# Optimization experiments

Hardware: AMD Instinct MI355X
Metric: run time of the kernel (lower is better)

## Reference

```python
import jax, jax.numpy as jnp
import numpy as np

D = 2048          # n_embd
F = 1408          # moe_inter_dim
E = 8             # n_routed_experts
TOPK = 2          # n_activated_experts
N_SHARED = 2
ROUTE_SCALE = 1.0


def setup_inputs() -> dict:
    key = jax.random.key(0)
    ks = jax.random.split(key, 8)
    s = 0.02
    x = jax.random.normal(ks[0], (2, 1024, D), dtype=jnp.float32)
    gate_w = jax.random.normal(ks[1], (D, E), dtype=jnp.float32) * s
    Fs = F * N_SHARED
    sw1 = jax.random.normal(ks[2], (D, Fs), dtype=jnp.float32) * s
    sw2 = jax.random.normal(ks[3], (Fs, D), dtype=jnp.float32) * s
    sw3 = jax.random.normal(ks[4], (D, Fs), dtype=jnp.float32) * s
    rw1 = jax.random.normal(ks[5], (E, D, F), dtype=jnp.float32) * s
    rw2 = jax.random.normal(ks[6], (E, F, D), dtype=jnp.float32) * s
    rw3 = jax.random.normal(ks[7], (E, D, F), dtype=jnp.float32) * s
    return {"x": x, "gate_w": gate_w, "sw1": sw1, "sw2": sw2, "sw3": sw3,
            "rw1": rw1, "rw2": rw2, "rw3": rw3}


def _swiglu(x, w1, w2, w3):
    return (jax.nn.silu(x @ w1) * (x @ w3)) @ w2


def reference(x, gate_w, sw1, sw2, sw3, rw1, rw2, rw3):
    B, T, _ = x.shape
    xf = x.reshape(-1, D)                       # [N, D]
    N = xf.shape[0]
    # shared experts (always applied)
    y = _swiglu(xf, sw1, sw2, sw3)              # [N, D]
    # gate: softmax scores, top-k (bias is None since n_embd != 7168; n_groups == 1)
    scores = jax.nn.softmax(xf @ gate_w, axis=-1)       # [N, E]
    weights, indices = jax.lax.top_k(scores, TOPK)       # gathered original scores
    weights = weights * ROUTE_SCALE
    # combine weights per (token, expert); zero for unassigned -> same math as
    # the per-expert gather/scatter loop in the original module
    cw = jnp.zeros((N, E), dtype=xf.dtype).at[jnp.arange(N)[:, None], indices].add(weights)
    for e in range(E):  # fixed small structural loop over experts
        h = _swiglu(xf, rw1[e], rw2[e], rw3[e])  # [N, D]
        y = y + cw[:, e:e + 1] * h
    return y.reshape(B, T, D)
```

## Files before the change

### kernel.cpp

```cpp
#include <hip/hip_runtime.h>
#include <hip/hip_bf16.h>
#include <math.h>

#define D_DIM 2048
#define F_DIM 1408
#define FS_DIM 2816
#define E_NUM 8
#define N_TOK 2048

typedef __attribute__((ext_vector_type(8))) short bf16x8;
typedef __attribute__((ext_vector_type(4))) float f32x4;

#define WAITVM(n) asm volatile("s_waitcnt vmcnt(" #n ")" ::: "memory")

__device__ inline short f2bf(float f) {
    __hip_bfloat16 h = __float2bfloat16(f);
    return *reinterpret_cast<short*>(&h);
}
__device__ inline float bf2f(short s) {
    __hip_bfloat16 h; *reinterpret_cast<short*>(&h) = s;
    return __bfloat162float(h);
}
__device__ inline float silu1(float v) { return v / (1.f + expf(-v)); }

__device__ inline void async_copy16(const void* g, void* l) {
    __builtin_amdgcn_global_load_lds(
        (const __attribute__((address_space(1))) void*)g,
        (__attribute__((address_space(3))) void*)l, 16, 0, 0);
}

#define SWZ(r, s) ((((s) ^ (((r) >> 1) & 3)) & 3) << 4)

__device__ inline void t64h(const float* in, short* out, int K, int N,
                            int kt, int nt, float (*tile)[65], int t)
{
    int k0 = kt * 64, n0 = nt * 64;
    int tr = t >> 4, tc4 = (t & 15) * 4;
#pragma unroll
    for (int i = 0; i < 4; ++i) {
        int r = tr + i * 16;
        float4 v = *reinterpret_cast<const float4*>(in + (size_t)(k0 + r) * N + n0 + tc4);
        tile[r][tc4 + 0] = v.x; tile[r][tc4 + 1] = v.y;
        tile[r][tc4 + 2] = v.z; tile[r][tc4 + 3] = v.w;
    }
    __syncthreads();
#pragma unroll
    for (int i = 0; i < 4; ++i) {
        int n = tr + i * 16;
        short4 s4;
        s4.x = f2bf(tile[tc4 + 0][n]);
        s4.y = f2bf(tile[tc4 + 1][n]);
        s4.z = f2bf(tile[tc4 + 2][n]);
        s4.w = f2bf(tile[tc4 + 3][n]);
        *reinterpret_cast<short4*>(out + (size_t)(n0 + n) * K + k0 + tc4) = s4;
    }
}

__global__ __launch_bounds__(256) void prep_kernel(
    const float* __restrict__ x, const float* __restrict__ gw,
    float* __restrict__ assign_w, int* __restrict__ expert_count,
    int* __restrict__ expert_list, short* __restrict__ Xb,
    const float* __restrict__ sw1, short* __restrict__ swt1,
    const float* __restrict__ sw3, short* __restrict__ swt3,
    const float* __restrict__ rw1, short* __restrict__ rwt1,
    const float* __restrict__ rw3, short* __restrict__ rwt3)
{
    __shared__ float tile[64][65];
    int bid = blockIdx.x;
    int tid = threadIdx.x;
    if (bid < 512) {
        int wid = bid * 4 + (tid >> 6);
        int lane = tid & 63;
        const float* xr = x + (size_t)wid * D_DIM;
        float p[E_NUM];
#pragma unroll
        for (int e = 0; e < E_NUM; ++e) p[e] = 0.f;
        for (int d = lane; d < D_DIM; d += 64) {
            float xv = xr[d];
            const float4* g = reinterpret_cast<const float4*>(gw + (size_t)d * E_NUM);
            float4 g0 = g[0], g1 = g[1];
            p[0] = fmaf(xv, g0.x, p[0]); p[1] = fmaf(xv, g0.y, p[1]);
            p[2] = fmaf(xv, g0.z, p[2]); p[3] = fmaf(xv, g0.w, p[3]);
            p[4] = fmaf(xv, g1.x, p[4]); p[5] = fmaf(xv, g1.y, p[5]);
            p[6] = fmaf(xv, g1.z, p[6]); p[7] = fmaf(xv, g1.w, p[7]);
        }
#pragma unroll
        for (int off = 32; off > 0; off >>= 1)
#pragma unroll
            for (int e = 0; e < E_NUM; ++e)
                p[e] += __shfl_xor(p[e], off, 64);
        if (lane == 0) {
            float m = p[0];
#pragma unroll
            for (int e = 1; e < E_NUM; ++e) m = fmaxf(m, p[e]);
            float s = 0.f, pr[E_NUM];
#pragma unroll
            for (int e = 0; e < E_NUM; ++e) { pr[e] = expf(p[e] - m); s += pr[e]; }
            float inv = 1.f / s;
#pragma unroll
            for (int e = 0; e < E_NUM; ++e) pr[e] *= inv;
            int i0 = 0;
#pragma unroll
            for (int e = 1; e < E_NUM; ++e) if (pr[e] > pr[i0]) i0 = e;
            int i1 = (i0 == 0) ? 1 : 0;
#pragma unroll
            for (int e = 0; e < E_NUM; ++e) if (e != i0 && pr[e] > pr[i1]) i1 = e;
            int s0 = wid * 2, s1 = wid * 2 + 1;
            assign_w[s0] = pr[i0];
            assign_w[s1] = pr[i1];
            int p0 = atomicAdd(&expert_count[i0], 1);
            expert_list[i0 * N_TOK + p0] = s0;
            int p1 = atomicAdd(&expert_count[i1], 1);
            expert_list[i1 * N_TOK + p1] = s1;
        }
    } else if (bid < 2560) {
        int i = ((bid - 512) * 256 + tid) * 8;
        float4 v0 = *reinterpret_cast<const float4*>(x + i);
        float4 v1 = *reinterpret_cast<const float4*>(x + i + 4);
        bf16x8 o;
        o[0] = f2bf(v0.x); o[1] = f2bf(v0.y); o[2] = f2bf(v0.z); o[3] = f2bf(v0.w);
        o[4] = f2bf(v1.x); o[5] = f2bf(v1.y); o[6] = f2bf(v1.z); o[7] = f2bf(v1.w);
        *reinterpret_cast<bf16x8*>(Xb + i) = o;
    } else if (bid < 3968) {
        int t = bid - 2560;
        t64h(sw1, swt1, D_DIM, FS_DIM, t % 32, t / 32, tile, tid);
    } else if (bid < 5376) {
        int t = bid - 3968;
        t64h(sw3, swt3, D_DIM, FS_DIM, t % 32, t / 32, tile, tid);
    } else if (bid < 11008) {
        int t = bid - 5376;
        int e = t / 704, r = t % 704;
        t64h(rw1 + (size_t)e * D_DIM * F_DIM, rwt1 + (size_t)e * F_DIM * D_DIM,
             D_DIM, F_DIM, r % 32, r / 32, tile, tid);
    } else {
        int t = bid - 11008;
        int e = t / 704, r = t % 704;
        t64h(rw3 + (size_t)e * D_DIM * F_DIM, rwt3 + (size_t)e * F_DIM * D_DIM,
             D_DIM, F_DIM, r % 32, r / 32, tile, tid);
    }
}

__global__ __launch_bounds__(256) void moe_in_kernel(
    const short* __restrict__ Xb,
    const short* __restrict__ swt1, const short* __restrict__ swt3, short* __restrict__ Hs,
    const short* __restrict__ rwt1, const short* __restrict__ rwt3, short* __restrict__ Hr,
    const int* __restrict__ expert_list, const int* __restrict__ expert_count,
    const float* __restrict__ sw2, short* __restrict__ swt2,
    const float* __restrict__ rw2, short* __restrict__ rwt2)
{
    __shared__ char SMEM[49152];
    int bid = blockIdx.x, tid = threadIdx.x;

    if (bid >= 3584) {
        int t2 = bid - 3584;
        float (*tile)[65] = reinterpret_cast<float (*)[65]>(SMEM);
        if (t2 < 1408) {
            t64h(sw2, swt2, FS_DIM, D_DIM, t2 % 44, t2 / 44, tile, tid);
        } else {
            int r = t2 - 1408;
            int e = r / 704, rr = r % 704;
            t64h(rw2 + (size_t)e * F_DIM * D_DIM, rwt2 + (size_t)e * D_DIM * F_DIM,
                 F_DIM, D_DIM, rr % 22, rr / 22, tile, tid);
        }
        return;
    }

    int xcd = bid & 7, qq = bid >> 3, mtile = qq & 15, gq = qq >> 4;
    int g = gq * 8 + xcd;
    if (g >= 220) return;
    bool gather;
    const short *W1, *W3;
    short* H;
    int ldH, n0, count;
    const int* list = nullptr;
    int m0 = mtile * 128;
    if (g < 44) {
        gather = false; count = N_TOK;
        W1 = swt1; W3 = swt3; H = Hs; ldH = FS_DIM; n0 = g * 64;
    } else {
        int g2 = g - 44, e = g2 / 22;
        n0 = (g2 % 22) * 64;
        gather = true;
        count = expert_count[e];
        if (m0 >= count) return;
        list = expert_list + e * N_TOK;
        W1 = rwt1 + (size_t)e * F_DIM * D_DIM;
        W3 = rwt3 + (size_t)e * F_DIM * D_DIM;
        H = Hr; ldH = F_DIM;
    }

    int l = tid & 63, w = tid >> 6;
    int wm = w >> 1, wn = w & 1, frow = l & 15, fkg = l >> 4;

    const char* aS[2];
#pragma unroll
    for (int j = 0; j < 2; ++j) {
        int u = j * 256 + tid, r = u >> 2, s = u & 3;
        int rr = m0 + r;
        int tok = gather ? ((rr < count) ? (list[rr] >> 1) : 0) : rr;
        aS[j] = (const char*)Xb + (size_t)tok * 4096 + SWZ(r, s);
    }
    int brr = tid >> 2, bss = tid & 3;
    size_t boff = (size_t)(n0 + brr) * 4096 + SWZ(brr, bss);
    const char* b1S = (const char*)W1 + boff;
    const char* b3S = (const char*)W3 + boff;

    f32x4 acc1[4][2], acc3[4][2];
#pragma unroll
    for (int i = 0; i < 4; ++i)
#pragma unroll
        for (int j = 0; j < 2; ++j) { acc1[i][j] = (f32x4)0.f; acc3[i][j] = (f32x4)0.f; }

#pragma unroll
    for (int p = 0; p < 2; ++p) {
        char* base = SMEM + p * 16384;
        int kb = p << 6;
        async_copy16(aS[0] + kb, base + tid * 16);
        async_copy16(aS[1] + kb, base + (256 + tid) * 16);
        async_copy16(b1S + kb, base + 8192 + tid * 16);
        async_copy16(b3S + kb, base + 12288 + tid * 16);
    }

    const int NIT = 64;
    for (int t = 0; t < NIT; ++t) {
        const char* base = SMEM + (t % 3) * 16384;
        WAITVM(4);
        __builtin_amdgcn_s_barrier();
        {
            int ts = (t + 2 < NIT) ? (t + 2) : (NIT - 1);
            char* sbase = SMEM + ((t + 2) % 3) * 16384;
            int skb = ts << 6;
            async_copy16(aS[0] + skb, sbase + tid * 16);
            async_copy16(aS[1] + skb, sbase + (256 + tid) * 16);
            async_copy16(b1S + skb, sbase + 8192 + tid * 16);
            async_copy16(b3S + skb, sbase + 12288 + tid * 16);
        }
        bf16x8 af[4], b1f[2], b3f[2];
#pragma unroll
        for (int mf = 0; mf < 4; ++mf) {
            int r = wm * 64 + mf * 16 + frow;
            af[mf] = *reinterpret_cast<const bf16x8*>(base + r * 64 + SWZ(r, fkg));
        }
#pragma unroll
        for (int nf = 0; nf < 2; ++nf) {
            int rb = wn * 32 + nf * 16 + frow;
            b1f[nf] = *reinterpret_cast<const bf16x8*>(base + 8192 + rb * 64 + SWZ(rb, fkg));
            b3f[nf] = *reinterpret_cast<const bf16x8*>(base + 12288 + rb * 64 + SWZ(rb, fkg));
        }
        __builtin_amdgcn_s_setprio(1);
#pragma unroll
        for (int mf = 0; mf < 4; ++mf)
#pragma unroll
            for (int nf = 0; nf < 2; ++nf) {
                acc1[mf][nf] = __builtin_amdgcn_mfma_f32_16x16x32_bf16(
                    af[mf], b1f[nf], acc1[mf][nf], 0, 0, 0);
                acc3[mf][nf] = __builtin_amdgcn_mfma_f32_16x16x32_bf16(
                    af[mf], b3f[nf], acc3[mf][nf], 0, 0, 0);
            }
        __builtin_amdgcn_s_setprio(0);
    }
    WAITVM(0);

#pragma unroll
    for (int mf = 0; mf < 4; ++mf) {
#pragma unroll
        for (int jj = 0; jj < 4; ++jj) {
            int rl = wm * 64 + mf * 16 + fkg * 4 + jj;
            int rr = m0 + rl;
            int s;
            if (gather) { if (rr >= count) continue; s = list[rr]; }
            else s = rr;
            short* hp = H + (size_t)s * ldH + n0 + wn * 32 + frow;
#pragma unroll
            for (int nf = 0; nf < 2; ++nf)
                hp[nf * 16] = f2bf(silu1(acc1[mf][nf][jj]) * acc3[mf][nf][jj]);
        }
    }
}

__global__ __launch_bounds__(256) void moe_out_kernel(
    const short* __restrict__ Hs, const short* __restrict__ swt2, float* __restrict__ Y,
    const short* __restrict__ Hr, const short* __restrict__ rwt2, short* __restrict__ H2,
    const int* __restrict__ expert_list, const int* __restrict__ expert_count)
{
    __shared__ char SMEM[49152];
    int bid = blockIdx.x, tid = threadIdx.x;
    int xcd = bid & 7, qq = bid >> 3, mtile = qq & 15, gq = qq >> 4;
    int g = gq * 8 + xcd;
    if (g >= 144) return;
    bool gather;
    const short *A, *B;
    int ldKb, NIT, n0, count;
    const int* list = nullptr;
    int m0 = mtile * 128;
    if (g < 16) {
        gather = false; count = N_TOK;
        A = Hs; ldKb = FS_DIM * 2; NIT = 88; B = swt2; n0 = g * 128;
    } else {
        int g2 = g - 16, e = g2 >> 4;
        n0 = (g2 & 15) * 128;
        gather = true;
        count = expert_count[e];
        if (m0 >= count) return;
        list = expert_list + e * N_TOK;
        A = Hr; ldKb = F_DIM * 2; NIT = 44;
        B = rwt2 + (size_t)e * D_DIM * F_DIM;
    }

    int l = tid & 63, w = tid >> 6;
    int wm = w >> 1, wn = w & 1, frow = l & 15, fkg = l >> 4;

    const char* aS[2];
#pragma unroll
    for (int j = 0; j < 2; ++j) {
        int u = j * 256 + tid, r = u >> 2, s = u & 3;
        int rr = m0 + r;
        int arow = gather ? ((rr < count) ? list[rr] : 0) : rr;
        aS[j] = (const char*)A + (size_t)arow * ldKb + SWZ(r, s);
    }
    const char* bS[2];
#pragma unroll
    for (int j = 0; j < 2; ++j) {
        int u = j * 256 + tid, r = u >> 2, s = u & 3;
        bS[j] = (const char*)B + (size_t)(n0 + r) * ldKb + SWZ(r, s);
    }

    f32x4 acc[4][4];
#pragma unroll
    for (int i = 0; i < 4; ++i)
#pragma unroll
        for (int j = 0; j < 4; ++j) acc[i][j] = (f32x4)0.f;

#pragma unroll
    for (int p = 0; p < 2; ++p) {
        char* base = SMEM + p * 16384;
        int kb = p << 6;
        async_copy16(aS[0] + kb, base + tid * 16);
        async_copy16(aS[1] + kb, base + (256 + tid) * 16);
        async_copy16(bS[0] + kb, base + 8192 + tid * 16);
        async_copy16(bS[1] + kb, base + 8192 + (256 + tid) * 16);
    }

    for (int t = 0; t < NIT; ++t) {
        const char* base = SMEM + (t % 3) * 16384;
        WAITVM(4);
        __builtin_amdgcn_s_barrier();
        {
            int ts = (t + 2 < NIT) ? (t + 2) : (NIT - 1);
            char* sbase = SMEM + ((t + 2) % 3) * 16384;
            int skb = ts << 6;
            async_copy16(aS[0] + skb, sbase + tid * 16);
            async_copy16(aS[1] + skb, sbase + (256 + tid) * 16);
            async_copy16(bS[0] + skb, sbase + 8192 + tid * 16);
            async_copy16(bS[1] + skb, sbase + 8192 + (256 + tid) * 16);
        }
        bf16x8 af[4], bf[4];
#pragma unroll
        for (int mf = 0; mf < 4; ++mf) {
            int r = wm * 64 + mf * 16 + frow;
            af[mf] = *reinterpret_cast<const bf16x8*>(base + r * 64 + SWZ(r, fkg));
        }
#pragma unroll
        for (int nf = 0; nf < 4; ++nf) {
            int rb = wn * 64 + nf * 16 + frow;
            bf[nf] = *reinterpret_cast<const bf16x8*>(base + 8192 + rb * 64 + SWZ(rb, fkg));
        }
        __builtin_amdgcn_s_setprio(1);
#pragma unroll
        for (int mf = 0; mf < 4; ++mf)
#pragma unroll
            for (int nf = 0; nf < 4; ++nf)
                acc[mf][nf] = __builtin_amdgcn_mfma_f32_16x16x32_bf16(
                    af[mf], bf[nf], acc[mf][nf], 0, 0, 0);
        __builtin_amdgcn_s_setprio(0);
    }
    WAITVM(0);

#pragma unroll
    for (int mf = 0; mf < 4; ++mf) {
#pragma unroll
        for (int jj = 0; jj < 4; ++jj) {
            int rl = wm * 64 + mf * 16 + fkg * 4 + jj;
            int rr = m0 + rl;
            int s;
            if (gather) { if (rr >= count) continue; s = list[rr]; }
            else s = rr;
            int col = n0 + wn * 64 + frow;
            if (!gather) {
                float* op = Y + (size_t)s * D_DIM + col;
#pragma unroll
                for (int nf = 0; nf < 4; ++nf)
                    op[nf * 16] = acc[mf][nf][jj];
            } else {
                short* op = H2 + (size_t)s * D_DIM + col;
#pragma unroll
                for (int nf = 0; nf < 4; ++nf)
                    op[nf * 16] = f2bf(acc[mf][nf][jj]);
            }
        }
    }
}

__global__ __launch_bounds__(256) void combine_kernel(
    float* __restrict__ Y, const short* __restrict__ H2,
    const float* __restrict__ assign_w)
{
    int tok = blockIdx.x, tid = threadIdx.x;
    float w0 = assign_w[2 * tok];
    float w1 = assign_w[2 * tok + 1];
    const short* h0 = H2 + (size_t)(2 * tok) * D_DIM + tid * 8;
    const short* h1 = h0 + D_DIM;
    bf16x8 a = *reinterpret_cast<const bf16x8*>(h0);
    bf16x8 b = *reinterpret_cast<const bf16x8*>(h1);
    float* y = Y + (size_t)tok * D_DIM + tid * 8;
    float4 y0 = *reinterpret_cast<float4*>(y);
    float4 y1 = *reinterpret_cast<float4*>(y + 4);
    y0.x = fmaf(w0, bf2f(a[0]), fmaf(w1, bf2f(b[0]), y0.x));
    y0.y = fmaf(w0, bf2f(a[1]), fmaf(w1, bf2f(b[1]), y0.y));
    y0.z = fmaf(w0, bf2f(a[2]), fmaf(w1, bf2f(b[2]), y0.z));
    y0.w = fmaf(w0, bf2f(a[3]), fmaf(w1, bf2f(b[3]), y0.w));
    y1.x = fmaf(w0, bf2f(a[4]), fmaf(w1, bf2f(b[4]), y1.x));
    y1.y = fmaf(w0, bf2f(a[5]), fmaf(w1, bf2f(b[5]), y1.y));
    y1.z = fmaf(w0, bf2f(a[6]), fmaf(w1, bf2f(b[6]), y1.z));
    y1.w = fmaf(w0, bf2f(a[7]), fmaf(w1, bf2f(b[7]), y1.w));
    *reinterpret_cast<float4*>(y) = y0;
    *reinterpret_cast<float4*>(y + 4) = y1;
}

extern "C" void kernel_launch(void* const* d_in, const int* in_sizes, int n_in,
                              void* d_out, int out_size, void* d_ws, size_t ws_size,
                              hipStream_t stream) {
    const float* x   = (const float*)d_in[0];
    const float* gw  = (const float*)d_in[1];
    const float* sw1 = (const float*)d_in[2];
    const float* sw2 = (const float*)d_in[3];
    const float* sw3 = (const float*)d_in[4];
    const float* rw1 = (const float*)d_in[5];
    const float* rw2 = (const float*)d_in[6];
    const float* rw3 = (const float*)d_in[7];
    float* Y = (float*)d_out;

    char* ws = (char*)d_ws;
    float* assign_w     = (float*)(ws);
    int*   expert_count = (int*)(ws + 16384);
    int*   expert_list  = (int*)(ws + 16384 + 256);

    const size_t XB_OFF   = 131072;
    const size_t SWT1_OFF = XB_OFF + 8388608ull;
    const size_t SWT3_OFF = SWT1_OFF + 11534336ull;
    const size_t SWT2_OFF = SWT3_OFF + 11534336ull;
    const size_t RWT1_OFF = SWT2_OFF + 11534336ull;
    const size_t RWT3_OFF = RWT1_OFF + 46137344ull;
    const size_t RWT2_OFF = RWT3_OFF + 46137344ull;
    const size_t HS_OFF   = RWT2_OFF + 46137344ull;
    const size_t HR_OFF   = HS_OFF + 11534336ull;
    const size_t H2_OFF   = HR_OFF + 11534336ull;

    short* Xb   = (short*)(ws + XB_OFF);
    short* swt1 = (short*)(ws + SWT1_OFF);
    short* swt3 = (short*)(ws + SWT3_OFF);
    short* swt2 = (short*)(ws + SWT2_OFF);
    short* rwt1 = (short*)(ws + RWT1_OFF);
    short* rwt3 = (short*)(ws + RWT3_OFF);
    short* rwt2 = (short*)(ws + RWT2_OFF);
    short* Hs   = (short*)(ws + HS_OFF);
    short* Hr   = (short*)(ws + HR_OFF);
    short* H2   = (short*)(ws + H2_OFF);

    hipMemsetAsync(expert_count, 0, E_NUM * sizeof(int), stream);

    prep_kernel<<<16640, 256, 0, stream>>>(
        x, gw, assign_w, expert_count, expert_list, Xb,
        sw1, swt1, sw3, swt3, rw1, rwt1, rw3, rwt3);

    moe_in_kernel<<<10624, 256, 0, stream>>>(
        Xb, swt1, swt3, Hs, rwt1, rwt3, Hr,
        expert_list, expert_count, sw2, swt2, rw2, rwt2);

    moe_out_kernel<<<2304, 256, 0, stream>>>(
        Hs, swt2, Y, Hr, rwt2, H2, expert_list, expert_count);

    combine_kernel<<<N_TOK, 256, 0, stream>>>(Y, H2, assign_w);
}
```

Measured before the change: 368.6 us.

## Widen moe_in tile to 128 columns and move w2 transposes into prep kernel

The gate/up GEMM kernel now computes 128x128 output tiles instead of 128x64. Each block loads a larger B slice and holds twice the accumulators, which improves reuse of the A operand and halves the number of GEMM blocks. The w2 transpose blocks move from moe_in_kernel into prep_kernel, so the GEMM kernel no longer carries mixed transpose work. In exchange, the larger LDS footprint (72KB) and extra accumulator registers may cut occupancy, and the fewer blocks may leave CUs underused for sparsely routed experts.

```diff
diff --git a/kernel.cpp b/kernel.cpp
--- a/kernel.cpp
+++ b/kernel.cpp
@@ -63,7 +63,9 @@
     const float* __restrict__ sw1, short* __restrict__ swt1,
     const float* __restrict__ sw3, short* __restrict__ swt3,
     const float* __restrict__ rw1, short* __restrict__ rwt1,
-    const float* __restrict__ rw3, short* __restrict__ rwt3)
+    const float* __restrict__ rw3, short* __restrict__ rwt3,
+    const float* __restrict__ sw2, short* __restrict__ swt2,
+    const float* __restrict__ rw2, short* __restrict__ rwt2)
 {
     __shared__ float tile[64][65];
     int bid = blockIdx.x;
@@ -132,11 +134,19 @@
         int e = t / 704, r = t % 704;
         t64h(rw1 + (size_t)e * D_DIM * F_DIM, rwt1 + (size_t)e * F_DIM * D_DIM,
              D_DIM, F_DIM, r % 32, r / 32, tile, tid);
-    } else {
+    } else if (bid < 16640) {
         int t = bid - 11008;
         int e = t / 704, r = t % 704;
         t64h(rw3 + (size_t)e * D_DIM * F_DIM, rwt3 + (size_t)e * F_DIM * D_DIM,
              D_DIM, F_DIM, r % 32, r / 32, tile, tid);
+    } else if (bid < 18048) {
+        int t = bid - 16640;
+        t64h(sw2, swt2, FS_DIM, D_DIM, t % 44, t / 44, tile, tid);
+    } else {
+        int t = bid - 18048;
+        int e = t / 704, r = t % 704;
+        t64h(rw2 + (size_t)e * F_DIM * D_DIM, rwt2 + (size_t)e * D_DIM * F_DIM,
+             F_DIM, D_DIM, r % 22, r / 22, tile, tid);
     }
 }
 
@@ -144,42 +154,25 @@
     const short* __restrict__ Xb,
     const short* __restrict__ swt1, const short* __restrict__ swt3, short* __restrict__ Hs,
     const short* __restrict__ rwt1, const short* __restrict__ rwt3, short* __restrict__ Hr,
-    const int* __restrict__ expert_list, const int* __restrict__ expert_count,
-    const float* __restrict__ sw2, short* __restrict__ swt2,
-    const float* __restrict__ rw2, short* __restrict__ rwt2)
+    const int* __restrict__ expert_list, const int* __restrict__ expert_count)
 {
-    __shared__ char SMEM[49152];
+    __shared__ char SMEM[73728];
     int bid = blockIdx.x, tid = threadIdx.x;
-
-    if (bid >= 3584) {
-        int t2 = bid - 3584;
-        float (*tile)[65] = reinterpret_cast<float (*)[65]>(SMEM);
-        if (t2 < 1408) {
-            t64h(sw2, swt2, FS_DIM, D_DIM, t2 % 44, t2 / 44, tile, tid);
-        } else {
-            int r = t2 - 1408;
-            int e = r / 704, rr = r % 704;
-            t64h(rw2 + (size_t)e * F_DIM * D_DIM, rwt2 + (size_t)e * D_DIM * F_DIM,
-                 F_DIM, D_DIM, rr % 22, rr / 22, tile, tid);
-        }
-        return;
-    }
-
     int xcd = bid & 7, qq = bid >> 3, mtile = qq & 15, gq = qq >> 4;
     int g = gq * 8 + xcd;
-    if (g >= 220) return;
+    if (g >= 110) return;
     bool gather;
     const short *W1, *W3;
     short* H;
     int ldH, n0, count;
     const int* list = nullptr;
     int m0 = mtile * 128;
-    if (g < 44) {
+    if (g < 22) {
         gather = false; count = N_TOK;
-        W1 = swt1; W3 = swt3; H = Hs; ldH = FS_DIM; n0 = g * 64;
+        W1 = swt1; W3 = swt3; H = Hs; ldH = FS_DIM; n0 = g * 128;
     } else {
-        int g2 = g - 44, e = g2 / 22;
-        n0 = (g2 % 22) * 64;
+        int g2 = g - 22, e = g2 / 11;
+        n0 = (g2 % 11) * 128;
         gather = true;
         count = expert_count[e];
         if (m0 >= count) return;
@@ -200,58 +193,66 @@
         int tok = gather ? ((rr < count) ? (list[rr] >> 1) : 0) : rr;
         aS[j] = (const char*)Xb + (size_t)tok * 4096 + SWZ(r, s);
     }
-    int brr = tid >> 2, bss = tid & 3;
-    size_t boff = (size_t)(n0 + brr) * 4096 + SWZ(brr, bss);
-    const char* b1S = (const char*)W1 + boff;
-    const char* b3S = (const char*)W3 + boff;
-
-    f32x4 acc1[4][2], acc3[4][2];
+    const char *b1S[2], *b3S[2];
+#pragma unroll
+    for (int j = 0; j < 2; ++j) {
+        int u = j * 256 + tid, r = u >> 2, s = u & 3;
+        size_t off = (size_t)(n0 + r) * 4096 + SWZ(r, s);
+        b1S[j] = (const char*)W1 + off;
+        b3S[j] = (const char*)W3 + off;
+    }
+
+    f32x4 acc1[4][4], acc3[4][4];
 #pragma unroll
     for (int i = 0; i < 4; ++i)
 #pragma unroll
-        for (int j = 0; j < 2; ++j) { acc1[i][j] = (f32x4)0.f; acc3[i][j] = (f32x4)0.f; }
+        for (int j = 0; j < 4; ++j) { acc1[i][j] = (f32x4)0.f; acc3[i][j] = (f32x4)0.f; }
 
 #pragma unroll
     for (int p = 0; p < 2; ++p) {
-        char* base = SMEM + p * 16384;
+        char* base = SMEM + p * 24576;
         int kb = p << 6;
         async_copy16(aS[0] + kb, base + tid * 16);
         async_copy16(aS[1] + kb, base + (256 + tid) * 16);
-        async_copy16(b1S + kb, base + 8192 + tid * 16);
-        async_copy16(b3S + kb, base + 12288 + tid * 16);
+        async_copy16(b1S[0] + kb, base + 8192 + tid * 16);
+        async_copy16(b1S[1] + kb, base + 8192 + (256 + tid) * 16);
+        async_copy16(b3S[0] + kb, base + 16384 + tid * 16);
+        async_copy16(b3S[1] + kb, base + 16384 + (256 + tid) * 16);
     }
 
     const int NIT = 64;
     for (int t = 0; t < NIT; ++t) {
-        const char* base = SMEM + (t % 3) * 16384;
-        WAITVM(4);
+        const char* base = SMEM + (t % 3) * 24576;
+        WAITVM(6);
         __builtin_amdgcn_s_barrier();
         {
             int ts = (t + 2 < NIT) ? (t + 2) : (NIT - 1);
-            char* sbase = SMEM + ((t + 2) % 3) * 16384;
+            char* sbase = SMEM + ((t + 2) % 3) * 24576;
             int skb = ts << 6;
             async_copy16(aS[0] + skb, sbase + tid * 16);
             async_copy16(aS[1] + skb, sbase + (256 + tid) * 16);
-            async_copy16(b1S + skb, sbase + 8192 + tid * 16);
-            async_copy16(b3S + skb, sbase + 12288 + tid * 16);
-        }
-        bf16x8 af[4], b1f[2], b3f[2];
+            async_copy16(b1S[0] + skb, sbase + 8192 + tid * 16);
+            async_copy16(b1S[1] + skb, sbase + 8192 + (256 + tid) * 16);
+            async_copy16(b3S[0] + skb, sbase + 16384 + tid * 16);
+            async_copy16(b3S[1] + skb, sbase + 16384 + (256 + tid) * 16);
+        }
+        bf16x8 af[4], b1f[4], b3f[4];
 #pragma unroll
         for (int mf = 0; mf < 4; ++mf) {
             int r = wm * 64 + mf * 16 + frow;
             af[mf] = *reinterpret_cast<const bf16x8*>(base + r * 64 + SWZ(r, fkg));
         }
 #pragma unroll
-        for (int nf = 0; nf < 2; ++nf) {
-            int rb = wn * 32 + nf * 16 + frow;
+        for (int nf = 0; nf < 4; ++nf) {
+            int rb = wn * 64 + nf * 16 + frow;
             b1f[nf] = *reinterpret_cast<const bf16x8*>(base + 8192 + rb * 64 + SWZ(rb, fkg));
-            b3f[nf] = *reinterpret_cast<const bf16x8*>(base + 12288 + rb * 64 + SWZ(rb, fkg));
+            b3f[nf] = *reinterpret_cast<const bf16x8*>(base + 16384 + rb * 64 + SWZ(rb, fkg));
         }
         __builtin_amdgcn_s_setprio(1);
 #pragma unroll
         for (int mf = 0; mf < 4; ++mf)
 #pragma unroll
-            for (int nf = 0; nf < 2; ++nf) {
+            for (int nf = 0; nf < 4; ++nf) {
                 acc1[mf][nf] = __builtin_amdgcn_mfma_f32_16x16x32_bf16(
                     af[mf], b1f[nf], acc1[mf][nf], 0, 0, 0);
                 acc3[mf][nf] = __builtin_amdgcn_mfma_f32_16x16x32_bf16(
@@ -270,9 +271,9 @@
             int s;
             if (gather) { if (rr >= count) continue; s = list[rr]; }
             else s = rr;
-            short* hp = H + (size_t)s * ldH + n0 + wn * 32 + frow;
-#pragma unroll
-            for (int nf = 0; nf < 2; ++nf)
+            short* hp = H + (size_t)s * ldH + n0 + wn * 64 + frow;
+#pragma unroll
+            for (int nf = 0; nf < 4; ++nf)
                 hp[nf * 16] = f2bf(silu1(acc1[mf][nf][jj]) * acc3[mf][nf][jj]);
         }
     }
@@ -469,13 +470,14 @@
 
     hipMemsetAsync(expert_count, 0, E_NUM * sizeof(int), stream);
 
-    prep_kernel<<<16640, 256, 0, stream>>>(
+    prep_kernel<<<23680, 256, 0, stream>>>(
         x, gw, assign_w, expert_count, expert_list, Xb,
-        sw1, swt1, sw3, swt3, rw1, rwt1, rw3, rwt3);
-
-    moe_in_kernel<<<10624, 256, 0, stream>>>(
+        sw1, swt1, sw3, swt3, rw1, rwt1, rw3, rwt3,
+        sw2, swt2, rw2, rwt2);
+
+    moe_in_kernel<<<1792, 256, 0, stream>>>(
         Xb, swt1, swt3, Hs, rwt1, rwt3, Hr,
-        expert_list, expert_count, sw2, swt2, rw2, rwt2);
+        expert_list, expert_count);
 
     moe_out_kernel<<<2304, 256, 0, stream>>>(
         Hs, swt2, Y, Hr, rwt2, H2, expert_list, expert_count);
```

Result: slower. 449.3 us (+21.9%).
